# Performance work log

Measured on AMD Instinct MI355X. Metric: run time of the kernel, lower is better.

## Reference

```python
import jax, jax.numpy as jnp
import numpy as np

B, N, C, S = 2, 250000, 32, 128


def setup_inputs() -> dict:
    key = jax.random.key(0)
    k1, k2, k3, k4 = jax.random.split(key, 4)
    # unique voxel coordinates per batch (spconv requires unique active sites)
    rng = np.random.default_rng(0)
    coords = []
    for b in range(B):
        lin = rng.choice(S * S * S, size=N, replace=False)
        x = lin // (S * S)
        y = (lin // S) % S
        z = lin % S
        coords.append(np.stack([x, y, z], axis=-1))
    coordinates = jnp.asarray(np.stack(coords, axis=0), dtype=jnp.int32)  # [B,N,3]
    features = jax.random.normal(k1, (B, N, C), dtype=jnp.float32)
    wscale = 1.0 / np.sqrt(27 * C)
    W1 = jax.random.normal(k2, (3, 3, 3, C, C), dtype=jnp.float32) * wscale
    W2 = jax.random.normal(k3, (3, 3, 3, C, C), dtype=jnp.float32) * wscale
    W3 = jax.random.normal(k4, (3, 3, 3, C, C), dtype=jnp.float32) * wscale
    return {
        "features": features,
        "coordinates": coordinates,
        "spatial_shape": jnp.array([S, S, S], dtype=jnp.int32),
        "batch_size": B,
        "W1": W1,
        "W2": W2,
        "W3": W3,
    }


def reference(features, coordinates, spatial_shape, batch_size, W1, W2, W3):
    Bs = int(batch_size)
    X, Y, Z = [int(s) for s in np.asarray(spatial_shape)]
    n = coordinates.shape[1]
    M = Bs * n
    cin = features.shape[-1]
    b_idx = jnp.repeat(jnp.arange(Bs, dtype=jnp.int32), n)  # [M]
    coords = coordinates.reshape(-1, 3).astype(jnp.int32)  # [M,3]
    feat = features.reshape(-1, cin)  # [M,Cin]
    # dense hash grid: voxel -> row index in feat, -1 if inactive
    grid = jnp.full((Bs, X, Y, Z), -1, dtype=jnp.int32)
    grid = grid.at[b_idx, coords[:, 0], coords[:, 1], coords[:, 2]].set(
        jnp.arange(M, dtype=jnp.int32))

    cx, cy, cz = coords[:, 0], coords[:, 1], coords[:, 2]

    def subm_conv(f, W):
        # submanifold 3x3x3 conv: output only at active sites, gather active
        # neighbors (rulebook gather -> GEMM -> accumulate)
        cout = W.shape[-1]
        out = jnp.zeros((M, cout), dtype=f.dtype)
        for dx in range(3):
            for dy in range(3):
                for dz in range(3):
                    nx, ny, nz = cx + dx - 1, cy + dy - 1, cz + dz - 1
                    valid = ((nx >= 0) & (nx < X) & (ny >= 0) & (ny < Y)
                             & (nz >= 0) & (nz < Z))
                    idx = grid[b_idx,
                               jnp.clip(nx, 0, X - 1),
                               jnp.clip(ny, 0, Y - 1),
                               jnp.clip(nz, 0, Z - 1)]
                    idx = jnp.where(valid, idx, -1)
                    g = jnp.where((idx >= 0)[:, None],
                                  f[jnp.maximum(idx, 0)], 0.0)
                    out = out + g @ W[dx, dy, dz]
        return out

    x = jax.nn.relu(subm_conv(feat, W1))
    x = jax.nn.relu(subm_conv(x, W2))
    x = subm_conv(x, W3)
    return x.reshape(Bs, n, -1)
```

## Files before the change

### kernel.cpp

```cpp
#include <hip/hip_runtime.h>

#define SG 128
#define C 32
#define NPB 250000
#define BATCH 2
#define M (BATCH * NPB)
#define MP 500032
#define NW (MP / 64)
#define NK 27
#define NBKT 65536
#define CAP 256
#define HSZ 512

typedef __attribute__((ext_vector_type(4))) float f32x4;
typedef __attribute__((ext_vector_type(8))) short bf16x8;

union frag_u { unsigned u[4]; bf16x8 v; };

__device__ __forceinline__ int bucket_key(int b, int x, int y, int z) {
    return (b << 15) | ((x >> 2) << 10) | ((y >> 2) << 5) | (z >> 2);
}

__device__ __forceinline__ void gl_lds16(const void* g, void* l) {
    __builtin_amdgcn_global_load_lds(
        (const __attribute__((address_space(1))) unsigned int*)g,
        (__attribute__((address_space(3))) unsigned int*)l, 16, 0, 0);
}

__device__ __forceinline__ void split1(float v, unsigned short& h, unsigned short& lo) {
    unsigned u = __float_as_uint(v);
    h = (unsigned short)(u >> 16);
    float hf = __uint_as_float(u & 0xFFFF0000u);
    lo = (unsigned short)(__float_as_uint(v - hf) >> 16);
}

__global__ void hist_kernel(const int* __restrict__ coords, int* __restrict__ hist) {
    int p = blockIdx.x * blockDim.x + threadIdx.x;
    if (p >= M) return;
    int x = coords[3 * p + 0], y = coords[3 * p + 1], z = coords[3 * p + 2];
    atomicAdd(&hist[bucket_key(p >= NPB, x, y, z)], 1);
}

__global__ __launch_bounds__(256) void scan1_kernel(int* __restrict__ h, int* __restrict__ bsum) {
    __shared__ int s[256];
    int t = threadIdx.x, b = blockIdx.x;
    int v = h[b * 256 + t];
    s[t] = v;
    __syncthreads();
    for (int off = 1; off < 256; off <<= 1) {
        int x = (t >= off) ? s[t - off] : 0;
        __syncthreads();
        s[t] += x;
        __syncthreads();
    }
    h[b * 256 + t] = s[t] - v;
    if (t == 255) bsum[b] = s[255];
}
__global__ __launch_bounds__(256) void scan2_kernel(int* __restrict__ bsum) {
    __shared__ int s[256];
    int t = threadIdx.x;
    int v = bsum[t];
    s[t] = v;
    __syncthreads();
    for (int off = 1; off < 256; off <<= 1) {
        int x = (t >= off) ? s[t - off] : 0;
        __syncthreads();
        s[t] += x;
        __syncthreads();
    }
    bsum[t] = s[t] - v;
}
__global__ __launch_bounds__(256) void scan3_kernel(int* __restrict__ h, const int* __restrict__ bsum) {
    h[blockIdx.x * 256 + threadIdx.x] += bsum[blockIdx.x];
}

__global__ void place_kernel(const int* __restrict__ coords, const float* __restrict__ f,
                             int* __restrict__ h, int* __restrict__ ord,
                             int* __restrict__ gridP, unsigned short* __restrict__ fpk) {
    int p = blockIdx.x * blockDim.x + threadIdx.x;
    if (p >= M) return;
    int x = coords[3 * p + 0], y = coords[3 * p + 1], z = coords[3 * p + 2];
    int b = (p >= NPB) ? 1 : 0;
    int j = atomicAdd(&h[bucket_key(b, x, y, z)], 1);
    ord[j] = p;
    gridP[((b * SG + x) * SG + y) * SG + z] = j;
    const f32x4* src = (const f32x4*)(f + (size_t)p * 32);
    unsigned short* dst = fpk + (size_t)j * 64;
#pragma unroll
    for (int c4 = 0; c4 < 8; c4++) {
        f32x4 v = src[c4];
        ushort4 hh, lo;
        split1(v[0], hh.x, lo.x);
        split1(v[1], hh.y, lo.y);
        split1(v[2], hh.z, lo.z);
        split1(v[3], hh.w, lo.w);
        *(ushort4*)(dst + c4 * 4) = hh;
        *(ushort4*)(dst + 32 + c4 * 4) = lo;
    }
}

__global__ __launch_bounds__(64) void build_dedup_kernel(
    const int* __restrict__ coords, const int* __restrict__ ord,
    const int* __restrict__ gridP,
    unsigned char* __restrict__ nbL, int* __restrict__ uniq, int* __restrict__ ucnt)
{
    __shared__ int hkey[HSZ];
    __shared__ int hval[HSZ];
    __shared__ int hcnt;
    const int t = threadIdx.x;
    const int w = blockIdx.x;
    for (int i = t; i < HSZ; i += 64) { hkey[i] = -2; hval[i] = -1; }
    if (t == 0) { hcnt = 65; uniq[w * CAP] = -1; }
    __syncthreads();

    const int j = w * 64 + t;
    int x = 0, y = 0, z = 0, base = 0;
    const bool real = (j < M);
    if (real) {
        int p = ord[j];
        x = coords[3 * p + 0]; y = coords[3 * p + 1]; z = coords[3 * p + 2];
        base = (p >= NPB) ? SG * SG * SG : 0;
    }

    if (real) {
        unsigned h = (((unsigned)j * 2654435761u) >> 20) & (HSZ - 1);
        for (;;) {
            int old = atomicCAS(&hkey[h], -2, j);
            if (old == -2) { hval[h] = 1 + t; uniq[w * CAP + 1 + t] = j; break; }
            h = (h + 1) & (HSZ - 1);
        }
    } else {
        uniq[w * CAP + 1 + t] = -1;
    }
    __syncthreads();

    for (int k = 0; k < NK; k++) {
        int slot = 0;
        if (k == 13) {
            slot = real ? (1 + t) : 0;
        } else {
            int id = -1;
            if (real) {
                int nx = x + k / 9 - 1;
                int ny = y + (k / 3) % 3 - 1;
                int nz = z + (k % 3) - 1;
                if ((unsigned)nx < SG && (unsigned)ny < SG && (unsigned)nz < SG)
                    id = gridP[base + (nx * SG + ny) * SG + nz];
            }
            if (id >= 0) {
                unsigned h = (((unsigned)id * 2654435761u) >> 20) & (HSZ - 1);
                slot = -1;
                while (slot < 0) {
                    int old = atomicCAS(&hkey[h], -2, id);
                    bool won = (old == -2);
                    int myslot = -1;
                    if (won) myslot = atomicAdd(&hcnt, 1);
                    if (won) {
                        if (myslot < CAP) { hval[h] = myslot; uniq[w * CAP + myslot] = id; slot = myslot; }
                        else { hval[h] = 0; slot = 0; }
                    } else if (old == id) {
                        int v = hval[h];
                        if (v >= 0) slot = v;
                    } else {
                        h = (h + 1) & (HSZ - 1);
                    }
                }
            }
        }
        nbL[((size_t)w * NK + k) * 64 + (t & 15) * 4 + (t >> 4)] = (unsigned char)slot;
    }
    __syncthreads();
    if (t == 0) ucnt[w] = (hcnt < CAP) ? hcnt : CAP;
}

__global__ void prep_w_kernel(const float* __restrict__ W1, const float* __restrict__ W2,
                              const float* __restrict__ W3, unsigned short* __restrict__ wpk) {
    int id = blockIdx.x * blockDim.x + threadIdx.x;
    if (id >= 3 * NK * 2 * 64) return;
    int which = id / (NK * 128);
    int rid = id - which * (NK * 128);
    const float* W = which == 0 ? W1 : which == 1 ? W2 : W3;
    unsigned short* wout = wpk + (size_t)which * NK * 2048;
    int l = rid & 63, ct = (rid >> 6) & 1, k = rid >> 7;
    int lrow = l & 15, kg = l >> 4;
    unsigned hw[4], lw[4];
#pragma unroll
    for (int jp = 0; jp < 4; jp++) {
        float v0 = W[k * 1024 + (kg * 8 + 2 * jp + 0) * 32 + ct * 16 + lrow];
        float v1 = W[k * 1024 + (kg * 8 + 2 * jp + 1) * 32 + ct * 16 + lrow];
        unsigned u0 = __float_as_uint(v0), u1 = __float_as_uint(v1);
        hw[jp] = (u0 >> 16) | (u1 & 0xFFFF0000u);
        float h0 = __uint_as_float(u0 & 0xFFFF0000u);
        float h1 = __uint_as_float(u1 & 0xFFFF0000u);
        lw[jp] = (__float_as_uint(v0 - h0) >> 16) | (__float_as_uint(v1 - h1) & 0xFFFF0000u);
    }
    unsigned* dh = (unsigned*)(wout + k * 2048 + ((ct * 2 + 0) * 64 + l) * 8);
    unsigned* dl = (unsigned*)(wout + k * 2048 + ((ct * 2 + 1) * 64 + l) * 8);
#pragma unroll
    for (int i = 0; i < 4; i++) { dh[i] = hw[i]; dl[i] = lw[i]; }
}

template <bool RELU, bool LAST>
__global__ __launch_bounds__(256) void conv_mfma(
    const unsigned short* __restrict__ fpk,
    const unsigned char* __restrict__ nbL,
    const int* __restrict__ uniq,
    const int* __restrict__ ucnt,
    const unsigned short* __restrict__ wpk,
    const unsigned short* __restrict__ zrow,
    const int* __restrict__ ord,
    unsigned short* __restrict__ opk,
    float* __restrict__ of32)
{
    __shared__ char bufA[CAP * 128];

    const int t = threadIdx.x;
    const int l = t & 63;
    const int wv = t >> 6;
    const int lrow = l & 15, kg = l >> 4;
    const int w = blockIdx.x;
    const int wbase = w * 64;

    const int lane_r = l >> 3;
    const int lc = l & 7;
    const int cnt = ucnt[w];
    {
        const int nneed = cnt - wv * 64;
        char* ldsb = bufA + wv * 64 * 128;
#pragma unroll
        for (int i = 0; i < 8; i++) {
            if (i * 8 < nneed) {
                int r = wv * 64 + i * 8 + lane_r;
                int id = (r < cnt) ? uniq[(size_t)w * CAP + r] : -1;
                const unsigned short* src = (id >= 0)
                    ? fpk + (size_t)id * 64 + ((lc ^ lane_r) << 3)
                    : zrow + (lc << 3);
                gl_lds16(src, ldsb + i * 1024);
            }
        }
    }

    const int kbeg = wv * 7;
    const int ntap = (wv == 3) ? 6 : 7;
    unsigned q[7];
#pragma unroll
    for (int i = 0; i < 7; i++) {
        int k = kbeg + i; if (k > 26) k = 26;
        q[i] = *(const unsigned*)(nbL + ((size_t)w * NK + k) * 64 + lrow * 4);
    }
    __builtin_amdgcn_sched_barrier(0);
    __syncthreads();

    f32x4 acc[4][2];
#pragma unroll
    for (int rt = 0; rt < 4; rt++)
#pragma unroll
        for (int ct = 0; ct < 2; ct++) acc[rt][ct] = (f32x4){0.f, 0.f, 0.f, 0.f};

#define LOADW(DST, K) { \
    const unsigned short* wb_ = wpk + ((K) << 11); \
    DST[0].v = *(const bf16x8*)(wb_ + ((0 * 64 + l) << 3)); \
    DST[1].v = *(const bf16x8*)(wb_ + ((1 * 64 + l) << 3)); \
    DST[2].v = *(const bf16x8*)(wb_ + ((2 * 64 + l) << 3)); \
    DST[3].v = *(const bf16x8*)(wb_ + ((3 * 64 + l) << 3)); }

#define TAP(I, WCUR, WNXT) \
    if ((I) < ntap) { \
        if ((I) + 1 < ntap) LOADW(WNXT, kbeg + (I) + 1); \
        int rows[4] = {(int)(q[I] & 255), (int)((q[I] >> 8) & 255), \
                       (int)((q[I] >> 16) & 255), (int)(q[I] >> 24)}; \
        frag_u ah[4], al[4]; \
        _Pragma("unroll") \
        for (int rt = 0; rt < 4; rt++) { \
            int r = rows[rt]; \
            const char* rb = bufA + (r << 7); \
            int sw = (r & 7) << 4; \
            ah[rt].v = *(const bf16x8*)(rb + ((kg << 4) ^ sw)); \
            al[rt].v = *(const bf16x8*)(rb + (((kg + 4) << 4) ^ sw)); \
        } \
        _Pragma("unroll") \
        for (int rt = 0; rt < 4; rt++) acc[rt][0] = __builtin_amdgcn_mfma_f32_16x16x32_bf16(ah[rt].v, WCUR[0].v, acc[rt][0], 0, 0, 0); \
        _Pragma("unroll") \
        for (int rt = 0; rt < 4; rt++) acc[rt][1] = __builtin_amdgcn_mfma_f32_16x16x32_bf16(ah[rt].v, WCUR[2].v, acc[rt][1], 0, 0, 0); \
        _Pragma("unroll") \
        for (int rt = 0; rt < 4; rt++) acc[rt][0] = __builtin_amdgcn_mfma_f32_16x16x32_bf16(ah[rt].v, WCUR[1].v, acc[rt][0], 0, 0, 0); \
        _Pragma("unroll") \
        for (int rt = 0; rt < 4; rt++) acc[rt][1] = __builtin_amdgcn_mfma_f32_16x16x32_bf16(ah[rt].v, WCUR[3].v, acc[rt][1], 0, 0, 0); \
        _Pragma("unroll") \
        for (int rt = 0; rt < 4; rt++) acc[rt][0] = __builtin_amdgcn_mfma_f32_16x16x32_bf16(al[rt].v, WCUR[0].v, acc[rt][0], 0, 0, 0); \
        _Pragma("unroll") \
        for (int rt = 0; rt < 4; rt++) acc[rt][1] = __builtin_amdgcn_mfma_f32_16x16x32_bf16(al[rt].v, WCUR[2].v, acc[rt][1], 0, 0, 0); \
    }

    frag_u wA[4], wB[4];
    LOADW(wA, kbeg);
    TAP(0, wA, wB); TAP(1, wB, wA); TAP(2, wA, wB); TAP(3, wB, wA);
    TAP(4, wA, wB); TAP(5, wB, wA); TAP(6, wA, wB);
#undef TAP
#undef LOADW

    __syncthreads();

    f32x4* dmp = (f32x4*)bufA;
#pragma unroll
    for (int rt = 0; rt < 4; rt++)
#pragma unroll
        for (int ct = 0; ct < 2; ct++)
            dmp[((wv * 8 + rt * 2 + ct) << 6) + l] = acc[rt][ct];
    __syncthreads();

    f32x4 fin[2] = {(f32x4){0.f, 0.f, 0.f, 0.f}, (f32x4){0.f, 0.f, 0.f, 0.f}};
#pragma unroll
    for (int s = 0; s < 4; s++)
#pragma unroll
        for (int ct = 0; ct < 2; ct++)
            fin[ct] += dmp[((s * 8 + wv * 2 + ct) << 6) + l];

    const int rbase = wbase + wv * 16 + 4 * kg;
#pragma unroll
    for (int j = 0; j < 4; j++) {
        int row = rbase + j;
        if (row < M) {
            int orow = LAST ? ord[row] : row;
#pragma unroll
            for (int ct = 0; ct < 2; ct++) {
                int col = ct * 16 + lrow;
                float v = fin[ct][j];
                if (RELU) v = fmaxf(v, 0.f);
                if (LAST) {
                    of32[orow * 32 + col] = v;
                } else {
                    unsigned short h, lo;
                    split1(v, h, lo);
                    opk[row * 64 + col] = h;
                    opk[row * 64 + 32 + col] = lo;
                }
            }
        }
    }
}

extern "C" void kernel_launch(void* const* d_in, const int* in_sizes, int n_in,
                              void* d_out, int out_size, void* d_ws, size_t ws_size,
                              hipStream_t stream) {
    const float* features    = (const float*)d_in[0];
    const int*   coordinates = (const int*)d_in[1];
    const float* W1 = (const float*)d_in[4];
    const float* W2 = (const float*)d_in[5];
    const float* W3 = (const float*)d_in[6];

    char* ws = (char*)d_ws;
    const size_t GRID_BYTES = (size_t)BATCH * SG * SG * SG * 4;
    const size_t NBL_BYTES  = (size_t)NW * NK * 64;
    const size_t UNIQ_BYTES = (size_t)NW * CAP * 4;
    const size_t UCNT_BYTES = (size_t)NW * 4;
    const size_t HIST_BYTES = (size_t)NBKT * 4;
    const size_t BSUM_BYTES = 256 * 4;
    const size_t ORD_BYTES  = (size_t)MP * 4;
    const size_t WPK_BYTES  = (size_t)NK * 2048 * 2;
    const size_t Z_BYTES    = 256;

    size_t off = 0;
    int* gridP = (int*)(ws + off); off += GRID_BYTES;
    unsigned char* nbL = (unsigned char*)(ws + off); off += NBL_BYTES;
    int* uniq  = (int*)(ws + off); off += UNIQ_BYTES;
    int* ucnt  = (int*)(ws + off); off += UCNT_BYTES;
    int* hist  = (int*)(ws + off); off += HIST_BYTES;
    int* bsum  = (int*)(ws + off); off += BSUM_BYTES;
    int* ord   = (int*)(ws + off); off += ORD_BYTES;
    unsigned short* wpk = (unsigned short*)(ws + off); off += 3 * WPK_BYTES;
    unsigned short* zrow = (unsigned short*)(ws + off); off += Z_BYTES;
    unsigned short* fpk_a = (unsigned short*)(ws + off); off += (size_t)MP * 64 * 2;
    unsigned short* fpk_b = (unsigned short*)d_out;
    float* out = (float*)d_out;
    unsigned short* wpk1 = wpk;
    unsigned short* wpk2 = wpk + NK * 2048;
    unsigned short* wpk3 = wpk + 2 * NK * 2048;

    hipMemsetAsync(gridP, 0xFF, GRID_BYTES, stream);
    hipMemsetAsync(hist, 0, HIST_BYTES, stream);
    hipMemsetAsync(zrow, 0, Z_BYTES, stream);

    hist_kernel<<<(M + 255) / 256, 256, 0, stream>>>(coordinates, hist);
    scan1_kernel<<<256, 256, 0, stream>>>(hist, bsum);
    scan2_kernel<<<1, 256, 0, stream>>>(bsum);
    scan3_kernel<<<256, 256, 0, stream>>>(hist, bsum);
    place_kernel<<<(M + 255) / 256, 256, 0, stream>>>(coordinates, features, hist, ord, gridP, fpk_a);
    build_dedup_kernel<<<NW, 64, 0, stream>>>(coordinates, ord, gridP, nbL, uniq, ucnt);

    const int PW = 3 * NK * 2 * 64;
    prep_w_kernel<<<(PW + 255) / 256, 256, 0, stream>>>(W1, W2, W3, wpk);

    conv_mfma<true,  false><<<NW, 256, 0, stream>>>(fpk_a, nbL, uniq, ucnt, wpk1, zrow, ord, fpk_b, nullptr);
    conv_mfma<true,  false><<<NW, 256, 0, stream>>>(fpk_b, nbL, uniq, ucnt, wpk2, zrow, ord, fpk_a, nullptr);
    conv_mfma<false, true ><<<NW, 256, 0, stream>>>(fpk_a, nbL, uniq, ucnt, wpk3, zrow, ord, nullptr, out);
}
```

Baseline: 378.4 us.

## Fold scan3 into place, batch dedup waves, shortcut self-tile neighbors

After: 389.4 us. +2.9%, slower.

```diff
diff --git a/kernel.cpp b/kernel.cpp
--- a/kernel.cpp
+++ b/kernel.cpp
@@ -70,18 +70,17 @@
     }
     bsum[t] = s[t] - v;
 }
-__global__ __launch_bounds__(256) void scan3_kernel(int* __restrict__ h, const int* __restrict__ bsum) {
-    h[blockIdx.x * 256 + threadIdx.x] += bsum[blockIdx.x];
-}
 
 __global__ void place_kernel(const int* __restrict__ coords, const float* __restrict__ f,
-                             int* __restrict__ h, int* __restrict__ ord,
+                             int* __restrict__ h, const int* __restrict__ bsum,
+                             int* __restrict__ ord,
                              int* __restrict__ gridP, unsigned short* __restrict__ fpk) {
     int p = blockIdx.x * blockDim.x + threadIdx.x;
     if (p >= M) return;
     int x = coords[3 * p + 0], y = coords[3 * p + 1], z = coords[3 * p + 2];
     int b = (p >= NPB) ? 1 : 0;
-    int j = atomicAdd(&h[bucket_key(b, x, y, z)], 1);
+    int key = bucket_key(b, x, y, z);
+    int j = atomicAdd(&h[key], 1) + bsum[key >> 8];
     ord[j] = p;
     gridP[((b * SG + x) * SG + y) * SG + z] = j;
     const f32x4* src = (const f32x4*)(f + (size_t)p * 32);
@@ -99,78 +98,80 @@
     }
 }
 
-__global__ __launch_bounds__(64) void build_dedup_kernel(
+__global__ __launch_bounds__(256) void build_dedup_kernel(
     const int* __restrict__ coords, const int* __restrict__ ord,
     const int* __restrict__ gridP,
     unsigned char* __restrict__ nbL, int* __restrict__ uniq, int* __restrict__ ucnt)
 {
-    __shared__ int hkey[HSZ];
-    __shared__ int hval[HSZ];
-    __shared__ int hcnt;
+    __shared__ int hkey[4][HSZ];
+    __shared__ int hval[4][HSZ];
+    __shared__ int hcnt[4];
     const int t = threadIdx.x;
-    const int w = blockIdx.x;
-    for (int i = t; i < HSZ; i += 64) { hkey[i] = -2; hval[i] = -1; }
-    if (t == 0) { hcnt = 65; uniq[w * CAP] = -1; }
-    __syncthreads();
-
-    const int j = w * 64 + t;
+    const int l = t & 63;
+    const int wv = t >> 6;
+    const int w = blockIdx.x * 4 + wv;
+    const bool active = (w < NW);
+
+    for (int i = l; i < HSZ; i += 64) { hkey[wv][i] = -2; hval[wv][i] = -1; }
+    if (l == 0) hcnt[wv] = 65;
+    __syncthreads();
+
+    const int j = w * 64 + l;
     int x = 0, y = 0, z = 0, base = 0;
-    const bool real = (j < M);
+    const bool real = active && (j < M);
     if (real) {
         int p = ord[j];
         x = coords[3 * p + 0]; y = coords[3 * p + 1]; z = coords[3 * p + 2];
         base = (p >= NPB) ? SG * SG * SG : 0;
     }
-
-    if (real) {
-        unsigned h = (((unsigned)j * 2654435761u) >> 20) & (HSZ - 1);
-        for (;;) {
-            int old = atomicCAS(&hkey[h], -2, j);
-            if (old == -2) { hval[h] = 1 + t; uniq[w * CAP + 1 + t] = j; break; }
-            h = (h + 1) & (HSZ - 1);
-        }
-    } else {
-        uniq[w * CAP + 1 + t] = -1;
-    }
-    __syncthreads();
-
-    for (int k = 0; k < NK; k++) {
-        int slot = 0;
-        if (k == 13) {
-            slot = real ? (1 + t) : 0;
-        } else {
-            int id = -1;
-            if (real) {
-                int nx = x + k / 9 - 1;
-                int ny = y + (k / 3) % 3 - 1;
-                int nz = z + (k % 3) - 1;
-                if ((unsigned)nx < SG && (unsigned)ny < SG && (unsigned)nz < SG)
-                    id = gridP[base + (nx * SG + ny) * SG + nz];
-            }
-            if (id >= 0) {
-                unsigned h = (((unsigned)id * 2654435761u) >> 20) & (HSZ - 1);
-                slot = -1;
-                while (slot < 0) {
-                    int old = atomicCAS(&hkey[h], -2, id);
-                    bool won = (old == -2);
-                    int myslot = -1;
-                    if (won) myslot = atomicAdd(&hcnt, 1);
-                    if (won) {
-                        if (myslot < CAP) { hval[h] = myslot; uniq[w * CAP + myslot] = id; slot = myslot; }
-                        else { hval[h] = 0; slot = 0; }
-                    } else if (old == id) {
-                        int v = hval[h];
-                        if (v >= 0) slot = v;
+    if (active) {
+        uniq[w * CAP + 1 + l] = real ? j : -1;
+        if (l == 0) uniq[w * CAP] = -1;
+    }
+
+    if (active) {
+        for (int k = 0; k < NK; k++) {
+            int slot = 0;
+            if (k == 13) {
+                slot = real ? (1 + l) : 0;
+            } else {
+                int id = -1;
+                if (real) {
+                    int nx = x + k / 9 - 1;
+                    int ny = y + (k / 3) % 3 - 1;
+                    int nz = z + (k % 3) - 1;
+                    if ((unsigned)nx < SG && (unsigned)ny < SG && (unsigned)nz < SG)
+                        id = gridP[base + (nx * SG + ny) * SG + nz];
+                }
+                if (id >= 0) {
+                    if ((id >> 6) == w) {
+                        slot = 1 + (id & 63);
                     } else {
-                        h = (h + 1) & (HSZ - 1);
+                        unsigned h = (((unsigned)id * 2654435761u) >> 20) & (HSZ - 1);
+                        slot = -1;
+                        while (slot < 0) {
+                            int old = atomicCAS(&hkey[wv][h], -2, id);
+                            bool won = (old == -2);
+                            int myslot = -1;
+                            if (won) myslot = atomicAdd(&hcnt[wv], 1);
+                            if (won) {
+                                if (myslot < CAP) { hval[wv][h] = myslot; uniq[w * CAP + myslot] = id; slot = myslot; }
+                                else { hval[wv][h] = 0; slot = 0; }
+                            } else if (old == id) {
+                                int v = hval[wv][h];
+                                if (v >= 0) slot = v;
+                            } else {
+                                h = (h + 1) & (HSZ - 1);
+                            }
+                        }
                     }
                 }
             }
+            nbL[((size_t)w * NK + k) * 64 + (l & 15) * 4 + (l >> 4)] = (unsigned char)slot;
         }
-        nbL[((size_t)w * NK + k) * 64 + (t & 15) * 4 + (t >> 4)] = (unsigned char)slot;
-    }
-    __syncthreads();
-    if (t == 0) ucnt[w] = (hcnt < CAP) ? hcnt : CAP;
+    }
+    __syncthreads();
+    if (active && l == 0) ucnt[w] = (hcnt[wv] < CAP) ? hcnt[wv] : CAP;
 }
 
 __global__ void prep_w_kernel(const float* __restrict__ W1, const float* __restrict__ W2,
@@ -304,17 +305,19 @@
     f32x4* dmp = (f32x4*)bufA;
 #pragma unroll
     for (int rt = 0; rt < 4; rt++)
+        if (rt != wv)
+#pragma unroll
+            for (int ct = 0; ct < 2; ct++)
+                dmp[((wv * 8 + rt * 2 + ct) << 6) + l] = acc[rt][ct];
+    __syncthreads();
+
+    f32x4 fin[2] = {(f32x4){0.f, 0.f, 0.f, 0.f}, (f32x4){0.f, 0.f, 0.f, 0.f}};
+#pragma unroll
+    for (int s = 0; s < 4; s++)
 #pragma unroll
         for (int ct = 0; ct < 2; ct++)
-            dmp[((wv * 8 + rt * 2 + ct) << 6) + l] = acc[rt][ct];
-    __syncthreads();
-
-    f32x4 fin[2] = {(f32x4){0.f, 0.f, 0.f, 0.f}, (f32x4){0.f, 0.f, 0.f, 0.f}};
-#pragma unroll
-    for (int s = 0; s < 4; s++)
-#pragma unroll
-        for (int ct = 0; ct < 2; ct++)
-            fin[ct] += dmp[((s * 8 + wv * 2 + ct) << 6) + l];
+            fin[ct] += (s == wv) ? acc[s][ct]
+                                 : dmp[((s * 8 + wv * 2 + ct) << 6) + l];
 
     const int rbase = wbase + wv * 16 + 4 * kg;
 #pragma unroll
@@ -384,9 +387,8 @@
     hist_kernel<<<(M + 255) / 256, 256, 0, stream>>>(coordinates, hist);
     scan1_kernel<<<256, 256, 0, stream>>>(hist, bsum);
     scan2_kernel<<<1, 256, 0, stream>>>(bsum);
-    scan3_kernel<<<256, 256, 0, stream>>>(hist, bsum);
-    place_kernel<<<(M + 255) / 256, 256, 0, stream>>>(coordinates, features, hist, ord, gridP, fpk_a);
-    build_dedup_kernel<<<NW, 64, 0, stream>>>(coordinates, ord, gridP, nbL, uniq, ucnt);
+    place_kernel<<<(M + 255) / 256, 256, 0, stream>>>(coordinates, features, hist, bsum, ord, gridP, fpk_a);
+    build_dedup_kernel<<<(NW + 3) / 4, 256, 0, stream>>>(coordinates, ord, gridP, nbL, uniq, ucnt);
 
     const int PW = 3 * NK * 2 * 64;
     prep_w_kernel<<<(PW + 255) / 256, 256, 0, stream>>>(W1, W2, W3, wpk);
```
